# Performance work log

Hardware: AMD Instinct MI355X
Metric: run time of the kernel (lower is better)

## Reference

```python
import jax, jax.numpy as jnp
import numpy as np

EMBED_DIM = 1024
N_HEADS = 16
HEAD_DIM = EMBED_DIM // N_HEADS

def setup_inputs() -> dict:
    key = jax.random.key(0)
    kx, kq, kk, kv, ko = jax.random.split(key, 5)
    s = 1.0 / np.sqrt(EMBED_DIM)
    return {
        "x": jax.random.normal(kx, (4, 2048, EMBED_DIM), dtype=jnp.float32),
        "Wq": jax.random.normal(kq, (EMBED_DIM, EMBED_DIM), dtype=jnp.float32) * s,
        "Wk": jax.random.normal(kk, (EMBED_DIM, EMBED_DIM), dtype=jnp.float32) * s,
        "Wv": jax.random.normal(kv, (EMBED_DIM, EMBED_DIM), dtype=jnp.float32) * s,
        "Wo": jax.random.normal(ko, (EMBED_DIM, EMBED_DIM), dtype=jnp.float32) * s,
    }

def reference(x, Wq, Wk, Wv, Wo):
    B, T, D = x.shape
    H, Dh = N_HEADS, HEAD_DIM
    # projections (nn.Linear: y = x @ W.T); split heads -> [B, H, T, Dh]
    Q = (x @ Wq.T).reshape(B, T, H, Dh).transpose(0, 2, 1, 3)
    K = (x @ Wk.T).reshape(B, T, H, Dh).transpose(0, 2, 1, 3)
    V = (x @ Wv.T).reshape(B, T, H, Dh).transpose(0, 2, 1, 3)
    scores = jnp.einsum("bhqd,bhkd->bhqk", Q, K) / jnp.sqrt(jnp.float32(Dh))
    attn = jax.nn.softmax(scores, axis=-1)
    out = jnp.einsum("bhqk,bhkd->bhqd", attn, V)  # [B,H,T,Dh]
    out = out.transpose(0, 2, 1, 3).reshape(B, T, D)
    return out @ Wo.T
```

## Files before the change

### kernel.cpp

```cpp
#include <hip/hip_runtime.h>

typedef _Float16 f16;
typedef _Float16 f16x8 __attribute__((ext_vector_type(8)));
typedef _Float16 f16x4 __attribute__((ext_vector_type(4)));
typedef float f32x4 __attribute__((ext_vector_type(4)));

#define MFMA16(a, b, c) __builtin_amdgcn_mfma_f32_16x16x32_f16((a), (b), (c), 0, 0, 0)
#define MEMBAR() __asm__ __volatile__("" ::: "memory")

__device__ __forceinline__ void cp16(const f16* g, f16* l) {
  __builtin_amdgcn_global_load_lds(
      (const __attribute__((address_space(1))) void*)g,
      (__attribute__((address_space(3))) void*)l, 16, 0, 0);
}

__global__ __launch_bounds__(256) void cvt_all(
    const float* __restrict__ x,  const float* __restrict__ Wq,
    const float* __restrict__ Wk, const float* __restrict__ Wv,
    const float* __restrict__ Wo,
    f16* __restrict__ X16, f16* __restrict__ Wq16, f16* __restrict__ Wk16,
    f16* __restrict__ Wv16, f16* __restrict__ Wo16) {
  int blk = blockIdx.x;
  const float* src; f16* dst; size_t off;
  if (blk < 4096) { src = x; dst = X16; off = (size_t)blk * 2048; }
  else {
    int t = blk - 4096, widx = t >> 9, loc = t & 511;
    src = (widx == 0) ? Wq : (widx == 1) ? Wk : (widx == 2) ? Wv : Wo;
    dst = (widx == 0) ? Wq16 : (widx == 1) ? Wk16 : (widx == 2) ? Wv16 : Wo16;
    off = (size_t)loc * 2048;
  }
  size_t e = off + (size_t)threadIdx.x * 8;
  const float4* s = (const float4*)(src + e);
  float4 a = s[0], b = s[1];
  f16x8 o;
  o[0] = (f16)a.x; o[1] = (f16)a.y; o[2] = (f16)a.z; o[3] = (f16)a.w;
  o[4] = (f16)b.x; o[5] = (f16)b.y; o[6] = (f16)b.z; o[7] = (f16)b.w;
  *(f16x8*)(dst + e) = o;
}

__device__ __forceinline__ void gemm_core(
    const f16* __restrict__ A, const f16* __restrict__ B, void* __restrict__ Cv,
    bool outF16, bool permT, int N, int K, int bm, int bn, float scale,
    f16* As, f16* Bs) {
  const int tid = threadIdx.x;
  const int lane = tid & 63, w = tid >> 6;
  const int wm = w >> 1, wn = w & 1;
  const int c = lane & 15, q = lane >> 4;
  const int key = (c >> 1) & 3;
  f32x4 acc[4][4] = {};

  const int Lrow = lane >> 2, Lp = (lane & 3) ^ ((lane >> 3) & 3);
  auto stage = [&](int k0, int bufi) {
#pragma unroll
    for (int j = 0; j < 2; ++j) {
      int r0 = (w * 2 + j) * 16;
      cp16(A + (size_t)(bm + r0 + Lrow) * K + k0 + Lp * 8,
           As + bufi * 4096 + r0 * 32 + lane * 8);
    }
#pragma unroll
    for (int j = 0; j < 2; ++j) {
      int r0 = (w * 2 + j) * 16;
      cp16(B + (size_t)(bn + r0 + Lrow) * K + k0 + Lp * 8,
           Bs + bufi * 4096 + r0 * 32 + lane * 8);
    }
  };

  stage(0, 0);
  const int NIT = K >> 5;
  for (int i = 0; i < NIT; ++i) {
    if (i + 1 < NIT) {
      stage((i + 1) << 5, (i + 1) & 1);
      __builtin_amdgcn_s_waitcnt(0x0F74);
    } else {
      __builtin_amdgcn_s_waitcnt(0x0F70);
    }
    __builtin_amdgcn_s_barrier();
    MEMBAR();
    const f16* Ab = As + (i & 1) * 4096;
    const f16* Bb = Bs + (i & 1) * 4096;
    f16x8 af[4], bf[4];
#pragma unroll
    for (int mt = 0; mt < 4; ++mt)
      af[mt] = *(const f16x8*)(Ab + (wm * 64 + mt * 16 + c) * 32 + (q ^ key) * 8);
#pragma unroll
    for (int nt = 0; nt < 4; ++nt)
      bf[nt] = *(const f16x8*)(Bb + (wn * 64 + nt * 16 + c) * 32 + (q ^ key) * 8);
#pragma unroll
    for (int mt = 0; mt < 4; ++mt)
#pragma unroll
      for (int nt = 0; nt < 4; ++nt)
        acc[mt][nt] = MFMA16(af[mt], bf[nt], acc[mt][nt]);
    MEMBAR();
    __builtin_amdgcn_s_barrier();
  }

#pragma unroll
  for (int mt = 0; mt < 4; ++mt)
#pragma unroll
    for (int nt = 0; nt < 4; ++nt)
#pragma unroll
      for (int r = 0; r < 4; ++r) {
        size_t row = bm + wm * 64 + mt * 16 + q * 4 + r;
        size_t col = bn + wn * 64 + nt * 16 + c;
        if (permT) {
          int t = (int)col & 63;
          col = (col & ~(size_t)63) |
                (size_t)((t & 0x23) | ((t & 0x0C) << 1) | ((t & 0x10) >> 2));
        }
        float v = acc[mt][nt][r] * scale;
        if (outF16) ((f16*)Cv)[row * N + col] = (f16)v;
        else ((float*)Cv)[row * N + col] = v;
      }
}

__global__ __launch_bounds__(256, 4) void gemm_qkvt(
    const f16* __restrict__ X, const f16* __restrict__ Wq,
    const f16* __restrict__ Wk, const f16* __restrict__ Wv,
    f16* __restrict__ Q, f16* __restrict__ Ko, f16* __restrict__ VT, float cs) {
  __shared__ __align__(16) f16 As[8192], Bs[8192];
  const int z = blockIdx.z, x = blockIdx.x;
  if (z < 2) {
    gemm_core(X, z ? Wk : Wq, z ? (void*)Ko : (void*)Q, true, false, 1024, 1024,
              (x >> 3) * 128, (x & 7) * 128, z ? 1.0f : cs, As, Bs);
  } else {
    gemm_core(Wv, X, (void*)VT, true, true, 8192, 1024,
              (x >> 6) * 128, (x & 63) * 128, 1.0f, As, Bs);
  }
}

__global__ __launch_bounds__(256, 4) void gemm_o(
    const f16* __restrict__ A, const f16* __restrict__ Wo, float* __restrict__ out) {
  __shared__ __align__(16) f16 As[8192], Bs[8192];
  const int x = blockIdx.x;
  gemm_core(A, Wo, (void*)out, false, false, 1024, 1024,
            (x >> 3) * 128, (x & 7) * 128, 1.0f, As, Bs);
}

__global__ __launch_bounds__(256, 2) void attn_kernel(
    const f16* __restrict__ Qg, const f16* __restrict__ Kg,
    const f16* __restrict__ VTg, f16* __restrict__ Og) {
  const int T = 2048, D = 1024;
  const int x = blockIdx.x;
  const int xcd = x & 7, rem = x >> 3;
  const int qt = rem & 7, grp = rem >> 3;
  const int bh = (grp << 3) | xcd;
  const int b = bh >> 4, h = bh & 15;
  const size_t base = ((size_t)b * T) * D + h * 64;
  const size_t baseV = (size_t)h * 64 * 8192 + (size_t)b * T;
  __shared__ __align__(16) f16 smem[24576];
  const int tid = threadIdx.x;
  const int lane = tid & 63, w = tid >> 6;
  const int c = lane & 15, q = lane >> 4;
  const int cx = c & 7;
  f16* Kb = smem;
  f16* Vb = smem + 12288;

#pragma unroll
  for (int j = 0; j < 8; ++j) {
    int cb = (w * 8 + j) * 64;
    int ch = cb + lane;
    int row = ch >> 3, p = (ch & 7) ^ (row & 7);
    cp16(Qg + base + (size_t)(qt * 256 + row) * D + p * 8, smem + cb * 8);
  }
  __syncthreads();
  f16x8 qf[4][2];
#pragma unroll
  for (int g = 0; g < 4; ++g)
#pragma unroll
    for (int kh = 0; kh < 2; ++kh)
      qf[g][kh] = *(const f16x8*)(smem + (w * 64 + g * 16 + c) * 64 + ((kh * 4 + q) ^ cx) * 8);
  __syncthreads();

  float l_[4] = {0.f, 0.f, 0.f, 0.f};
  f32x4 o_[4][4] = {};

  auto stageKV = [&](int kv, int bufi) {
    f16* Ks = Kb + bufi * 4096;
    f16* Vt = Vb + bufi * 4096;
#pragma unroll
    for (int j = 0; j < 2; ++j) {
      int cb = (w * 2 + j) * 64;
      int ch = cb + lane;
      int row = ch >> 3, p = (ch & 7) ^ (row & 7);
      cp16(Kg + base + (size_t)(kv + row) * D + p * 8, Ks + cb * 8);
    }
#pragma unroll
    for (int j = 0; j < 2; ++j) {
      int cb = (w * 2 + j) * 64;
      int ch = cb + lane;
      int row = ch >> 3, p = (ch & 7) ^ (row & 7);
      cp16(VTg + baseV + (size_t)row * 8192 + kv + p * 8, Vt + cb * 8);
    }
  };

  stageKV(0, 0);
  stageKV(64, 1);
  for (int i = 0; i < 32; ++i) {
    if (i < 31) __builtin_amdgcn_s_waitcnt(0x0F74);
    else        __builtin_amdgcn_s_waitcnt(0x0F70);
    __builtin_amdgcn_s_barrier();
    MEMBAR();
    if (i + 2 < 32) stageKV((i + 2) * 64, (i + 2) % 3);

    const f16* Ks = Kb + (i % 3) * 4096;
    const f16* Vt = Vb + (i % 3) * 4096;

    f32x4 st[4][4] = {};
#pragma unroll
    for (int kh = 0; kh < 2; ++kh) {
      f16x8 kf[4];
#pragma unroll
      for (int mt = 0; mt < 4; ++mt)
        kf[mt] = *(const f16x8*)(Ks + (mt * 16 + c) * 64 + ((kh * 4 + q) ^ cx) * 8);
      __builtin_amdgcn_s_setprio(1);
#pragma unroll
      for (int mt = 0; mt < 4; ++mt)
#pragma unroll
        for (int g = 0; g < 4; ++g)
          st[mt][g] = MFMA16(kf[mt], qf[g][kh], st[mt][g]);
      __builtin_amdgcn_s_setprio(0);
    }

    f16x8 pf[4][2];
#pragma unroll
    for (int g = 0; g < 4; ++g) {
      float s = 0.f;
#pragma unroll
      for (int mt = 0; mt < 4; ++mt) {
        float p0 = __builtin_amdgcn_exp2f(st[mt][g][0]);
        float p1 = __builtin_amdgcn_exp2f(st[mt][g][1]);
        float p2 = __builtin_amdgcn_exp2f(st[mt][g][2]);
        float p3 = __builtin_amdgcn_exp2f(st[mt][g][3]);
        s += (p0 + p1) + (p2 + p3);
        int kc = mt >> 1, hh = (mt & 1) * 4;
        pf[g][kc][hh + 0] = (f16)p0; pf[g][kc][hh + 1] = (f16)p1;
        pf[g][kc][hh + 2] = (f16)p2; pf[g][kc][hh + 3] = (f16)p3;
      }
      l_[g] += s;
    }

    __builtin_amdgcn_s_setprio(1);
#pragma unroll
    for (int kc = 0; kc < 2; ++kc)
#pragma unroll
      for (int d = 0; d < 4; ++d) {
        f16x8 vf = *(const f16x8*)(Vt + (d * 16 + c) * 64 + ((kc * 4 + q) ^ cx) * 8);
        o_[0][d] = MFMA16(pf[0][kc], vf, o_[0][d]);
        o_[1][d] = MFMA16(pf[1][kc], vf, o_[1][d]);
        o_[2][d] = MFMA16(pf[2][kc], vf, o_[2][d]);
        o_[3][d] = MFMA16(pf[3][kc], vf, o_[3][d]);
      }
    __builtin_amdgcn_s_setprio(0);
    MEMBAR();
  }

#pragma unroll
  for (int g = 0; g < 4; ++g) {
    l_[g] += __shfl_xor(l_[g], 16);
    l_[g] += __shfl_xor(l_[g], 32);
  }

#pragma unroll
  for (int g = 0; g < 4; ++g)
#pragma unroll
    for (int r = 0; r < 4; ++r) {
      float linv = 1.0f / __shfl(l_[g], q * 4 + r);
      size_t row = (size_t)qt * 256 + w * 64 + g * 16 + q * 4 + r;
#pragma unroll
      for (int d = 0; d < 4; ++d)
        Og[base + row * D + d * 16 + c] = (f16)(o_[g][d][r] * linv);
    }
}

extern "C" void kernel_launch(void* const* d_in, const int* in_sizes, int n_in,
                              void* d_out, int out_size, void* d_ws, size_t ws_size,
                              hipStream_t stream) {
  const float* x  = (const float*)d_in[0];
  const float* Wq = (const float*)d_in[1];
  const float* Wk = (const float*)d_in[2];
  const float* Wv = (const float*)d_in[3];
  const float* Wo = (const float*)d_in[4];
  char* ws = (char*)d_ws;
  const size_t MB = 1ull << 20;
  f16* X16  = (f16*)(ws + 0 * MB);
  f16* Wq16 = (f16*)(ws + 16 * MB);
  f16* Wk16 = (f16*)(ws + 18 * MB);
  f16* Wv16 = (f16*)(ws + 20 * MB);
  f16* Wo16 = (f16*)(ws + 22 * MB);
  f16* Q16  = (f16*)(ws + 24 * MB);
  f16* K16  = (f16*)(ws + 40 * MB);
  f16* VT16 = (f16*)(ws + 56 * MB);
  f16* A16  = (f16*)(ws + 72 * MB);

  const float cs = 0.18033688011112042f;

  cvt_all<<<6144, 256, 0, stream>>>(x, Wq, Wk, Wv, Wo,
                                    X16, Wq16, Wk16, Wv16, Wo16);

  gemm_qkvt<<<dim3(512, 1, 3), 256, 0, stream>>>(
      X16, Wq16, Wk16, Wv16, Q16, K16, VT16, cs);

  attn_kernel<<<dim3(512, 1, 1), 256, 0, stream>>>(Q16, K16, VT16, A16);

  gemm_o<<<512, 256, 0, stream>>>(A16, Wo16, (float*)d_out);
}
```

Before: 254.6 us.

## Software-pipeline QK^T of next KV tile with softmax and PV of current tile

Restructures the attention loop so the QK^T scores for tile i+1 are computed in the same iteration as the exp/softmax and PV MFMAs for tile i. The first tile's scores are produced in a prologue and the last tile's PV runs in an epilogue. The goal is to let the exp2 VALU work overlap with the score MFMAs and hide the LDS load latency of the K fragments. In exchange it holds the st and kf arrays live across iterations, which raises register pressure and could reduce occupancy. The loop now always waits for all outstanding copies (vmcnt 0) before each barrier, since it reads the newest staged tile one iteration early.

```diff
diff --git a/kernel.cpp b/kernel.cpp
--- a/kernel.cpp
+++ b/kernel.cpp
@@ -173,6 +173,7 @@
 
   float l_[4] = {0.f, 0.f, 0.f, 0.f};
   f32x4 o_[4][4] = {};
+  const f32x4 zero4 = {0.f, 0.f, 0.f, 0.f};
 
   auto stageKV = [&](int kv, int bufi) {
     f16* Ks = Kb + bufi * 4096;
@@ -193,33 +194,46 @@
     }
   };
 
+  auto loadKF = [&](const f16* Ks, f16x8 kf[2][4]) {
+#pragma unroll
+    for (int kh = 0; kh < 2; ++kh)
+#pragma unroll
+      for (int mt = 0; mt < 4; ++mt)
+        kf[kh][mt] = *(const f16x8*)(Ks + (mt * 16 + c) * 64 + ((kh * 4 + q) ^ cx) * 8);
+  };
+
+  f32x4 st[4][4];
+
   stageKV(0, 0);
   stageKV(64, 1);
-  for (int i = 0; i < 32; ++i) {
-    if (i < 31) __builtin_amdgcn_s_waitcnt(0x0F74);
-    else        __builtin_amdgcn_s_waitcnt(0x0F70);
+  __builtin_amdgcn_s_waitcnt(0x0F74);
+  __builtin_amdgcn_s_barrier();
+  MEMBAR();
+  {
+    f16x8 kf[2][4];
+    loadKF(Kb, kf);
+    __builtin_amdgcn_s_setprio(1);
+#pragma unroll
+    for (int mt = 0; mt < 4; ++mt)
+#pragma unroll
+      for (int g = 0; g < 4; ++g)
+        st[mt][g] = MFMA16(kf[0][mt], qf[g][0], zero4);
+#pragma unroll
+    for (int mt = 0; mt < 4; ++mt)
+#pragma unroll
+      for (int g = 0; g < 4; ++g)
+        st[mt][g] = MFMA16(kf[1][mt], qf[g][1], st[mt][g]);
+    __builtin_amdgcn_s_setprio(0);
+  }
+
+  for (int i = 0; i < 31; ++i) {
+    __builtin_amdgcn_s_waitcnt(0x0F70);
     __builtin_amdgcn_s_barrier();
     MEMBAR();
-    if (i + 2 < 32) stageKV((i + 2) * 64, (i + 2) % 3);
-
-    const f16* Ks = Kb + (i % 3) * 4096;
-    const f16* Vt = Vb + (i % 3) * 4096;
-
-    f32x4 st[4][4] = {};
-#pragma unroll
-    for (int kh = 0; kh < 2; ++kh) {
-      f16x8 kf[4];
-#pragma unroll
-      for (int mt = 0; mt < 4; ++mt)
-        kf[mt] = *(const f16x8*)(Ks + (mt * 16 + c) * 64 + ((kh * 4 + q) ^ cx) * 8);
-      __builtin_amdgcn_s_setprio(1);
-#pragma unroll
-      for (int mt = 0; mt < 4; ++mt)
-#pragma unroll
-        for (int g = 0; g < 4; ++g)
-          st[mt][g] = MFMA16(kf[mt], qf[g][kh], st[mt][g]);
-      __builtin_amdgcn_s_setprio(0);
-    }
+    if (i < 30) stageKV((i + 2) * 64, (i + 2) % 3);
+
+    f16x8 kf[2][4];
+    loadKF(Kb + ((i + 1) % 3) * 4096, kf);
 
     f16x8 pf[4][2];
 #pragma unroll
@@ -241,6 +255,18 @@
 
     __builtin_amdgcn_s_setprio(1);
 #pragma unroll
+    for (int mt = 0; mt < 4; ++mt)
+#pragma unroll
+      for (int g = 0; g < 4; ++g)
+        st[mt][g] = MFMA16(kf[0][mt], qf[g][0], zero4);
+#pragma unroll
+    for (int mt = 0; mt < 4; ++mt)
+#pragma unroll
+      for (int g = 0; g < 4; ++g)
+        st[mt][g] = MFMA16(kf[1][mt], qf[g][1], st[mt][g]);
+
+    const f16* Vt = Vb + (i % 3) * 4096;
+#pragma unroll
     for (int kc = 0; kc < 2; ++kc)
 #pragma unroll
       for (int d = 0; d < 4; ++d) {
@@ -252,6 +278,39 @@
       }
     __builtin_amdgcn_s_setprio(0);
     MEMBAR();
+  }
+
+  {
+    f16x8 pf[4][2];
+#pragma unroll
+    for (int g = 0; g < 4; ++g) {
+      float s = 0.f;
+#pragma unroll
+      for (int mt = 0; mt < 4; ++mt) {
+        float p0 = __builtin_amdgcn_exp2f(st[mt][g][0]);
+        float p1 = __builtin_amdgcn_exp2f(st[mt][g][1]);
+        float p2 = __builtin_amdgcn_exp2f(st[mt][g][2]);
+        float p3 = __builtin_amdgcn_exp2f(st[mt][g][3]);
+        s += (p0 + p1) + (p2 + p3);
+        int kc = mt >> 1, hh = (mt & 1) * 4;
+        pf[g][kc][hh + 0] = (f16)p0; pf[g][kc][hh + 1] = (f16)p1;
+        pf[g][kc][hh + 2] = (f16)p2; pf[g][kc][hh + 3] = (f16)p3;
+      }
+      l_[g] += s;
+    }
+    const f16* Vt = Vb + (31 % 3) * 4096;
+    __builtin_amdgcn_s_setprio(1);
+#pragma unroll
+    for (int kc = 0; kc < 2; ++kc)
+#pragma unroll
+      for (int d = 0; d < 4; ++d) {
+        f16x8 vf = *(const f16x8*)(Vt + (d * 16 + c) * 64 + ((kc * 4 + q) ^ cx) * 8);
+        o_[0][d] = MFMA16(pf[0][kc], vf, o_[0][d]);
+        o_[1][d] = MFMA16(pf[1][kc], vf, o_[1][d]);
+        o_[2][d] = MFMA16(pf[2][kc], vf, o_[2][d]);
+        o_[3][d] = MFMA16(pf[3][kc], vf, o_[3][d]);
+      }
+    __builtin_amdgcn_s_setprio(0);
   }
 
 #pragma unroll
```

Result: no change. 259.6 us (+1.9%).
